# Kernel optimization log

Measured on AMD Instinct MI355X. Metric: run time of the kernel, lower is better.

## Reference

```python
import jax, jax.numpy as jnp
import numpy as np

NUM_Q = 100000; NUM_C = 1000; D = 128; BS = 128; SEQ = 128
QN = 4; CN = 10; NQC = 4; AGG_HOPS = 2; RANK_K = 10
NEG = jnp.float32(-1e9)


def setup_inputs() -> dict:
    key = jax.random.key(0)
    ks = iter(jax.random.split(key, 40))
    def nrm(shape, scale=0.05):
        return jax.random.normal(next(ks), shape, dtype=jnp.float32) * scale
    inp = {}
    inp['question_seq'] = jax.random.randint(next(ks), (BS, SEQ), 0, NUM_Q, dtype=jnp.int32)
    inp['correct_seq'] = jax.random.randint(next(ks), (BS, SEQ), 0, 2, dtype=jnp.int32)
    inp['mask_seq'] = jnp.ones((BS, SEQ), dtype=jnp.int32)
    inp['question_neighbors'] = jax.random.randint(next(ks), (NUM_Q, QN), 0, NUM_C, dtype=jnp.int32)
    inp['concept_neighbors'] = jax.random.randint(next(ks), (NUM_C, CN), 0, NUM_Q, dtype=jnp.int32)
    inp['qc_table'] = jax.random.randint(next(ks), (NUM_Q, NQC), 0, NUM_C, dtype=jnp.int32)
    inp['Eq'] = nrm((NUM_Q, D), 1.0)
    inp['Ec'] = nrm((NUM_C, D), 1.0)
    inp['Er'] = nrm((2, D), 1.0)
    inp['W_ih1'] = nrm((3 * D, 2 * D)); inp['W_hh1'] = nrm((3 * D, D))
    inp['b_ih1'] = nrm((3 * D,)); inp['b_hh1'] = nrm((3 * D,))
    inp['W_ih2'] = nrm((3 * D, D)); inp['W_hh2'] = nrm((3 * D, D))
    inp['b_ih2'] = nrm((3 * D,)); inp['b_hh2'] = nrm((3 * D,))
    inp['W_agg'] = nrm((AGG_HOPS, D, D)); inp['b_agg'] = nrm((AGG_HOPS, D))
    inp['W_agg_last'] = nrm((D, D)); inp['b_agg_last'] = nrm((D,))
    inp['Wq'] = nrm((D, D)); inp['bq'] = nrm((D,))
    inp['Wk'] = nrm((D, D)); inp['bk'] = nrm((D,))
    inp['Ww'] = nrm((1, 2 * D)); inp['bw'] = nrm((1,))
    inp['h1_init'] = nrm((BS, D)); inp['h2_init'] = nrm((BS, D))
    return inp


def _gru(x, h, W_ih, W_hh, b_ih, b_hh):
    gi = x @ W_ih.T + b_ih
    gh = h @ W_hh.T + b_hh
    ir, iz, i_n = jnp.split(gi, 3, axis=-1)
    hr, hz, hn = jnp.split(gh, 3, axis=-1)
    r = jax.nn.sigmoid(ir + hr)
    z = jax.nn.sigmoid(iz + hz)
    n = jnp.tanh(i_n + r * hn)
    return (1 - z) * n + z * h


def _forward(question_seq, correct_seq, mask_seq, question_neighbors, concept_neighbors, qc_table,
             Eq, Ec, Er, W_ih1, W_hh1, b_ih1, b_hh1, W_ih2, W_hh2, b_ih2, b_hh2,
             W_agg, b_agg, W_agg_last, b_agg_last, Wq, bq, Wk, bk, Ww, bw, h1_init, h2_init):
    bs, seq_len = question_seq.shape
    d = Eq.shape[1]
    # detached question embeddings of the whole history (recap scoring key)
    K_all = jax.lax.stop_gradient(Eq[question_seq])  # [bs, seq, d]
    Wh, Wqc = Ww[:, :d], Ww[:, d:]  # MLP_W split over [state; question_concept]

    def predict(qc, hist, hist_mask):
        # qc: [bs,nqc,d], hist: [bs,ns,d], hist_mask: [bs,ns]
        Kp = qc @ Wk.T + bk                     # MLP_key
        Qp = hist @ Wq.T + bq                   # MLP_query
        logits = jnp.einsum('bsd,bqd->bsq', Qp, Kp)
        logits = jnp.where(hist_mask[:, :, None], logits, NEG)
        w = jax.nn.softmax(logits.reshape(bs, -1), axis=1)
        # pairwise sigmoid(MLP_W([h; e])) without materializing the concat
        v = jax.nn.sigmoid((hist @ Wh[0])[:, :, None] + (qc @ Wqc[0])[:, None, :] + bw[0])
        return jnp.sum(w * v.reshape(bs, -1), axis=1)

    def step(carry, t):
        h1, h2, state_hist, y_hat = carry
        q_t = jnp.take(question_seq, t, axis=1)
        r_t = jnp.take(correct_seq, t, axis=1)
        m_t = jnp.take(mask_seq, t, axis=1) != 0
        # --- 2-hop GNN aggregation (question -> concept -> question) ---
        n1 = question_neighbors[q_t]            # [bs, QN] concept ids
        n2 = concept_neighbors[n1]              # [bs, QN, CN] question ids
        emb = [Eq[q_t], Ec[n1], Eq[n2]]
        for i in range(AGG_HOPS):
            for j in range(AGG_HOPS - i):
                s = jnp.mean(emb[j + 1], axis=-2) + emb[j]
                emb[j] = jnp.tanh(s @ W_agg[j].T + b_agg[j])
        agg = jnp.tanh(emb[0] @ W_agg_last.T + b_agg_last)
        emb_q = jnp.where(m_t[:, None], agg, Eq[q_t])
        # --- GRU state updates (dropout in eval mode = identity) ---
        h1n = _gru(jnp.concatenate([emb_q, Er[r_t]], axis=1), h1, W_ih1, W_hh1, b_ih1, b_hh1)
        g2 = _gru(h1n, h2, W_ih2, W_hh2, b_ih2, b_hh2)
        # --- next question + its concepts ---
        q_next = jnp.take(question_seq, t + 1, axis=1)
        qc = jnp.concatenate([Eq[q_next][:, None], Ec[qc_table[q_next]]], axis=1)  # [bs, 1+NQC, d]
        # --- soft recap: top-k history states by detached embedding similarity ---
        scores = jnp.einsum('bsd,bd->bs', K_all, jax.lax.stop_gradient(Eq[q_next]))
        valid = jnp.arange(seq_len) < t
        scores = jnp.where(valid[None, :], scores, NEG)
        top_vals, top_idx = jax.lax.top_k(scores, RANK_K)
        sel = jnp.take_along_axis(state_hist, top_idx[:, :, None], axis=1)  # [bs, k, d]
        sel_mask = top_vals > NEG / 2
        hist = jnp.concatenate([g2[:, None], sel], axis=1)
        hist_mask = jnp.concatenate([jnp.ones((bs, 1), dtype=bool), sel_mask], axis=1)
        p = predict(qc, hist, hist_mask)
        idx = jnp.where(t == 0, 0, t + 1)  # original writes y_hat[:,0] at t==0
        y_hat = y_hat.at[:, idx].set(p)
        # h2 / state_history NOT updated at t==0 (original `continue`)
        upd = t > 0
        h2n = jnp.where(upd, g2, h2)
        state_hist = jnp.where(upd, state_hist.at[:, t].set(g2), state_hist)
        return (h1n, h2n, state_hist, y_hat), None

    init = (h1_init, h2_init,
            jnp.zeros((bs, seq_len, d), jnp.float32),
            jnp.zeros((bs, seq_len), jnp.float32))
    (_, _, _, y_hat), _ = jax.lax.scan(jax.checkpoint(step), init, jnp.arange(seq_len - 1))
    return y_hat


def reference(question_seq, correct_seq, mask_seq, question_neighbors, concept_neighbors, qc_table,
              Eq, Ec, Er, W_ih1, W_hh1, b_ih1, b_hh1, W_ih2, W_hh2, b_ih2, b_hh2,
              W_agg, b_agg, W_agg_last, b_agg_last, Wq, bq, Wk, bk, Ww, bw, h1_init, h2_init):
    return _forward(question_seq, correct_seq, mask_seq, question_neighbors, concept_neighbors, qc_table,
                    Eq, Ec, Er, W_ih1, W_hh1, b_ih1, b_hh1, W_ih2, W_hh2, b_ih2, b_hh2,
                    W_agg, b_agg, W_agg_last, b_agg_last, Wq, bq, Wk, bk, Ww, bw, h1_init, h2_init)
```

## Files before the change

kernel.cpp:

```cpp
#include <hip/hip_runtime.h>

#define DD 128
#define BSZ 128
#define SEQL 128
#define TST 127
#define QNN 4
#define CNN 10
#define NQCC 4
#define RKK 10
#define NEGV -1000000000.0f

#define OFF_WTA0    0
#define OFF_WTA1    16384
#define OFF_WTAL    32768
#define OFF_WTIH1A  49152
#define OFF_ERIH1   98304
#define OFF_MT      99072
#define OFF_WPACK   115456
#define OFF_ECA0    189184
#define OFF_E1C     317184
#define OFF_KQC     445184
#define OFF_VQCC    509184
#define OFF_KBC     510184
#define OFF_U       511184
#define OFF_W2      511312
#define OFF_C0      511440
#define OFF_GRAM    511488
#define OFF_GI1     511488
#define OFF_KQ0     6753792
#define OFF_VQC0    7802368
#define OFF_KB0     7818752
#define OFF_TIX     7835136
#define OFF_TMSK    7997696
#define OFF_CID     8160256

#define XI(e) ((e) + (((e) >> 5) << 2))
#define PH(e) ((((e) >> 5) * 40) + ((e) & 31))
#define PU(e) ((((e) >> 5) * 20) + (((e) & 31) >> 1))

typedef __fp16 h2 __attribute__((ext_vector_type(2)));

__device__ __forceinline__ float sigm(float x) { return 1.0f / (1.0f + __expf(-x)); }
__device__ __forceinline__ float ftanh(float x) {
  float ax = fabsf(x);
  float T = __expf(-2.f * ax);
  float r = (1.f - T) * __builtin_amdgcn_rcpf(1.f + T);
  return copysignf(r, x);
}
__device__ __forceinline__ unsigned pkh(float a, float b) {
  h2 v; v.x = (__fp16)a; v.y = (__fp16)b;
  return __builtin_bit_cast(unsigned, v);
}
__device__ __forceinline__ float fd2(float acc, unsigned w, h2 x) {
  return __builtin_amdgcn_fdot2(__builtin_bit_cast(h2, w), x, acc, false);
}
__device__ __forceinline__ float fd2u(float acc, unsigned w, unsigned x) {
  return __builtin_amdgcn_fdot2(__builtin_bit_cast(h2, w), __builtin_bit_cast(h2, x), acc, false);
}
__device__ __forceinline__ void bar() {
  asm volatile("s_waitcnt lgkmcnt(0)" ::: "memory");
  __builtin_amdgcn_s_barrier();
  asm volatile("" ::: "memory");
}

__global__ __launch_bounds__(256) void k_prep(
    const float* __restrict__ W_hh1, const float* __restrict__ W_ih2,
    const float* __restrict__ W_hh2, const float* __restrict__ W_agg,
    const float* __restrict__ W_agg_last, const float* __restrict__ W_ih1,
    const float* __restrict__ Er, const float* __restrict__ Wq,
    const float* __restrict__ Wk, const float* __restrict__ bq,
    const float* __restrict__ bk, float* __restrict__ ws) {
  int tid = threadIdx.x;
  if (blockIdx.x < 675) {
    int idx = blockIdx.x * 256 + tid;
    const int TOT = 172800;
    for (int o = idx; o < TOT; o += 675 * 256) {
      int r = o;
      if (r < 16384) { int j = r >> 7, i = r & 127; ws[OFF_WTA0 + r] = W_agg[i * 128 + j]; continue; }
      r -= 16384;
      if (r < 16384) { int j = r >> 7, i = r & 127; ws[OFF_WTA1 + r] = W_agg[16384 + i * 128 + j]; continue; }
      r -= 16384;
      if (r < 16384) { int j = r >> 7, i = r & 127; ws[OFF_WTAL + r] = W_agg_last[i * 128 + j]; continue; }
      r -= 16384;
      if (r < 49152) { int j = r / 384, i = r % 384; ws[OFF_WTIH1A + r] = W_ih1[i * 256 + j]; continue; }
      r -= 49152;
      if (r < 768) {
        int rr = r / 384, i2 = r % 384;
        float a = 0.f;
        for (int j = 0; j < 128; ++j) a += Er[rr * 128 + j] * W_ih1[i2 * 256 + 128 + j];
        ws[OFF_ERIH1 + r] = a; continue;
      }
      r -= 768;
      {
        int n = r & 3; int q = r >> 2;
        int i = q & 127; q >>= 7;
        int kk = q & 3; q >>= 2;
        int jc = q & 3; int c = q >> 2;
        int j0 = jc * 32 + kk * 8 + n * 2;
        const float* row;
        if (c < 3) row = W_hh1 + (size_t)(c * 128 + i) * 128;
        else if (c < 6) row = W_ih2 + (size_t)((c - 3) * 128 + i) * 128;
        else row = W_hh2 + (size_t)((c - 6) * 128 + i) * 128;
        ((unsigned*)ws)[OFF_WPACK + r] = pkh(row[j0], row[j0 + 1]);
      }
    }
  } else {
    int j = blockIdx.x - 675;
    __shared__ float wkc[128];
    __shared__ float sc[128];
    if (j < 128) {
      if (tid < 128) wkc[tid] = Wk[tid * 128 + j];
      __syncthreads();
      if (tid < 128) {
        float a = 0.f;
        for (int l = 0; l < 128; ++l) a = fmaf(Wq[l * 128 + tid], wkc[l], a);
        ws[OFF_MT + j * 128 + tid] = a;
      }
    } else if (j == 128) {
      if (tid < 128) {
        float a = 0.f;
        for (int l = 0; l < 128; ++l) a = fmaf(Wq[l * 128 + tid], bk[l], a);
        ws[OFF_U + tid] = a;
      }
    } else {
      if (tid < 128) {
        float a = 0.f;
        for (int l = 0; l < 128; ++l) a = fmaf(bq[l], Wk[l * 128 + tid], a);
        ws[OFF_W2 + tid] = a;
        sc[tid] = bq[tid] * bk[tid];
      }
      __syncthreads();
      if (tid == 0) { float s = 0.f; for (int l = 0; l < 128; ++l) s += sc[l]; ws[OFF_C0] = s; }
    }
  }
}

__global__ __launch_bounds__(128) void k_concept(
    const int* __restrict__ cnbr, const float* __restrict__ Eq,
    const float* __restrict__ Ec, const float* __restrict__ b_agg,
    const float* __restrict__ Ww, float* __restrict__ ws) {
  int c = blockIdx.x;
  int tid = threadIdx.x;
  __shared__ int s_nb[CNN];
  __shared__ float s_v[DD], s_ec[DD], s_t2[DD], s_w2[DD], s_kb2[DD];
  if (tid < CNN) s_nb[tid] = cnbr[c * CNN + tid];
  __syncthreads();
  float ec = Ec[c * DD + tid];
  float cm = 0.f;
#pragma unroll
  for (int l = 0; l < CNN; ++l) cm += Eq[(size_t)s_nb[l] * DD + tid];
  s_ec[tid] = ec;
  s_v[tid] = cm * 0.1f + ec;
  __syncthreads();
  const float* WtA0 = ws + OFF_WTA0;
  const float* WtA1 = ws + OFF_WTA1;
  const float* MT = ws + OFF_MT;
  float a1 = 0.f, a0 = 0.f, kq = 0.f;
#pragma unroll 8
  for (int j = 0; j < DD; ++j) {
    a1 += WtA1[j * DD + tid] * s_v[j];
    a0 += WtA0[j * DD + tid] * s_ec[j];
    kq += MT[j * DD + tid] * s_ec[j];
  }
  ws[OFF_E1C + c * DD + tid] = ftanh(a1 + b_agg[DD + tid]);
  ws[OFF_ECA0 + c * DD + tid] = a0;
  s_t2[tid] = kq + ws[OFF_U + tid];
  s_w2[tid] = s_ec[tid] * Ww[128 + tid];
  s_kb2[tid] = s_ec[tid] * ws[OFF_W2 + tid];
  __syncthreads();
  if (tid < 64) {
    ((unsigned*)ws)[OFF_KQC + c * 64 + tid] = pkh(s_t2[2 * tid], s_t2[2 * tid + 1]);
    float pa = s_w2[tid] + s_w2[tid + 64];
    float pb = s_kb2[tid] + s_kb2[tid + 64];
    for (int off = 32; off > 0; off >>= 1) { pa += __shfl_down(pa, off); pb += __shfl_down(pb, off); }
    if (tid == 0) { ws[OFF_VQCC + c] = pa; ws[OFF_KBC + c] = pb + ws[OFF_C0]; }
  }
}

__global__ __launch_bounds__(256) void k_gram(
    const int* __restrict__ qseq, const float* __restrict__ Eq,
    const float* __restrict__ Ww, float* __restrict__ ws) {
  int role = blockIdx.x >> 7;
  int b = blockIdx.x & 127;
  int tid = threadIdx.x;
  __shared__ float sX[128][129];
  __shared__ int sq[SEQL];
  if (tid < 128) sq[tid] = qseq[b * SEQL + tid];
  __syncthreads();
  for (int o = tid; o < 128 * 32; o += 256) {
    int s = o >> 5, p = o & 31;
    float4 v = ((const float4*)(Eq + (size_t)sq[s] * DD))[p];
    sX[s][p * 4] = v.x; sX[s][p * 4 + 1] = v.y; sX[s][p * 4 + 2] = v.z; sX[s][p * 4 + 3] = v.w;
  }
  __syncthreads();
  if (role == 0) {
    int r0 = (tid >> 4) * 8, c0 = (tid & 15) * 8;
    float acc[8][8];
#pragma unroll
    for (int u = 0; u < 8; ++u)
#pragma unroll
      for (int v = 0; v < 8; ++v) acc[u][v] = 0.f;
    for (int k = 0; k < 128; ++k) {
      float a[8], bb[8];
#pragma unroll
      for (int u = 0; u < 8; ++u) { a[u] = sX[r0 + u][k]; bb[u] = sX[c0 + u][k]; }
#pragma unroll
      for (int u = 0; u < 8; ++u)
#pragma unroll
        for (int v = 0; v < 8; ++v) acc[u][v] = fmaf(a[u], bb[v], acc[u][v]);
    }
    float* gb = ws + OFF_GRAM + (size_t)b * 16384;
#pragma unroll
    for (int u = 0; u < 8; ++u) {
      float4 v0 = {acc[u][0], acc[u][1], acc[u][2], acc[u][3]};
      float4 v1 = {acc[u][4], acc[u][5], acc[u][6], acc[u][7]};
      ((float4*)(gb + (size_t)(r0 + u) * 128 + c0))[0] = v0;
      ((float4*)(gb + (size_t)(r0 + u) * 128 + c0 + 4))[0] = v1;
    }
  } else {
    __shared__ float s_tmp[2][8][DD];
    __shared__ float sU[DD], sWqc[DD], sW2[DD];
    if (tid < 128) {
      sU[tid] = ws[OFF_U + tid];
      sWqc[tid] = Ww[128 + tid];
      sW2[tid] = ws[OFF_W2 + tid];
    }
    __syncthreads();
    const float* MT = ws + OFF_MT;
    unsigned* KQ0 = (unsigned*)ws + OFF_KQ0;
    int i = tid & 127, half = tid >> 7;
    int s0 = half * 64;
    for (int sb = 0; sb < 64; sb += 8) {
      float acc[8];
#pragma unroll
      for (int u = 0; u < 8; ++u) acc[u] = 0.f;
      for (int j = 0; j < DD; ++j) {
        float w = MT[j * DD + i];
#pragma unroll
        for (int u = 0; u < 8; ++u) acc[u] = fmaf(w, sX[s0 + sb + u][j], acc[u]);
      }
      __syncthreads();
#pragma unroll
      for (int u = 0; u < 8; ++u) s_tmp[half][u][i] = acc[u] + sU[i];
      __syncthreads();
      for (int o = tid; o < 16 * 64; o += 256) {
        int rr = o >> 6, e = o & 63;
        int hh = rr >> 3, uu = rr & 7;
        int s = hh * 64 + sb + uu;
        KQ0[((size_t)b * 128 + s) * 64 + e] = pkh(s_tmp[hh][uu][2 * e], s_tmp[hh][uu][2 * e + 1]);
      }
      __syncthreads();
    }
    if (tid < 128) {
      float a = 0.f, kb = 0.f;
      for (int j = 0; j < DD; ++j) {
        float xv = sX[tid][j];
        a = fmaf(xv, sWqc[j], a);
        kb = fmaf(xv, sW2[j], kb);
      }
      ws[OFF_VQC0 + b * 128 + tid] = a;
      ws[OFF_KB0 + b * 128 + tid] = kb + ws[OFF_C0];
    }
  }
}

__global__ __launch_bounds__(128) void k_topk(
    const int* __restrict__ qseq, const int* __restrict__ qctab,
    float* __restrict__ ws) {
  int* tix = (int*)(ws + OFF_TIX);
  int* tmsk = (int*)(ws + OFF_TMSK);
  int* cid = (int*)(ws + OFF_CID);
  int tid = threadIdx.x;
  int lane = tid & 63, wv = tid >> 6;
  int bt = blockIdx.x * 2 + wv;
  int b = bt / TST, t = bt - b * TST;
  if (lane < 5) {
    int qn = qseq[b * SEQL + t + 1];
    cid[(b * 128 + t + 1) * 5 + lane] = (lane == 0) ? qn : qctab[qn * NQCC + lane - 1];
  }
  const float* grow = ws + OFF_GRAM + ((size_t)b * 128 + (t + 1)) * 128;
  float v0 = (lane < t) ? grow[lane] : NEGV;
  float v1 = (lane + 64 < t) ? grow[lane + 64] : NEGV;
  for (int k = 0; k < RKK; ++k) {
    float bv = v0; int bi = lane;
    if (v1 > bv) { bv = v1; bi = lane + 64; }
    for (int off = 32; off > 0; off >>= 1) {
      float ov = __shfl_down(bv, off);
      int oi = __shfl_down(bi, off);
      if (ov > bv || (ov == bv && oi < bi)) { bv = ov; bi = oi; }
    }
    bv = __shfl(bv, 0); bi = __shfl(bi, 0);
    if (lane == 0) {
      tix[bt * RKK + k] = bi;
      tmsk[bt * RKK + k] = (bv > NEGV * 0.5f) ? 1 : 0;
    }
    if (bi == lane) v0 = -__builtin_inff();
    if (bi == lane + 64) v1 = -__builtin_inff();
  }
}

__global__ __launch_bounds__(128) void k_agg(
    const int* __restrict__ qseq, const int* __restrict__ rseq,
    const int* __restrict__ mseq, const int* __restrict__ qnbr,
    const float* __restrict__ Eq, const float* __restrict__ b_agg,
    const float* __restrict__ b_agg_last, const float* __restrict__ b_ih1,
    float* __restrict__ ws) {
  int blk = blockIdx.x;
  int b = blk >> 4, g = blk & 15;
  int t0 = g * 8;
  int nu = (t0 + 8 <= TST) ? 8 : (TST - t0);
  int tid = threadIdx.x;
  __shared__ float s_a[8][DD], s_b[8][DD], s_c[8][DD];
  __shared__ int s_q[8], s_r[8], s_m[8];
  __shared__ int s_n1[8][QNN];
  if (tid < 8) {
    int ok = tid < nu;
    int idx = b * SEQL + (ok ? (t0 + tid) : 0);
    s_q[tid] = qseq[idx];
    s_r[tid] = ok ? rseq[idx] : 0;
    s_m[tid] = ok ? mseq[idx] : 0;
  }
  __syncthreads();
  if (tid < 32) { int u = tid >> 2, k = tid & 3; s_n1[u][k] = qnbr[s_q[u] * QNN + k]; }
  for (int o = tid; o < 8 * 32; o += 128) {
    int u = o >> 5, p = o & 31;
    float4 v = ((const float4*)(Eq + (size_t)s_q[u] * DD))[p];
    s_a[u][p * 4] = v.x; s_a[u][p * 4 + 1] = v.y; s_a[u][p * 4 + 2] = v.z; s_a[u][p * 4 + 3] = v.w;
  }
  __syncthreads();
  const float* WtA0 = ws + OFF_WTA0;
  const float* WtAL = ws + OFF_WTAL;
  const float* WtIH1A = ws + OFF_WTIH1A;
  const float* EcA0 = ws + OFF_ECA0;
  const float* E1C = ws + OFF_E1C;
  float acc[8];
#pragma unroll
  for (int u = 0; u < 8; ++u) acc[u] = 0.f;
  for (int j = 0; j < DD; ++j) {
    float w = WtA0[j * DD + tid];
#pragma unroll
    for (int u = 0; u < 8; ++u) acc[u] = fmaf(w, s_a[u][j], acc[u]);
  }
  float bat = b_agg[tid];
#pragma unroll
  for (int u = 0; u < 8; ++u) {
    int n0 = s_n1[u][0], n1 = s_n1[u][1], n2 = s_n1[u][2], n3 = s_n1[u][3];
    float pre0 = 0.25f * (EcA0[n0 * DD + tid] + EcA0[n1 * DD + tid] + EcA0[n2 * DD + tid] + EcA0[n3 * DD + tid]);
    float e0 = ftanh(acc[u] + pre0 + bat);
    float e1m = 0.25f * (E1C[n0 * DD + tid] + E1C[n1 * DD + tid] + E1C[n2 * DD + tid] + E1C[n3 * DD + tid]);
    s_b[u][tid] = e1m + e0;
  }
  __syncthreads();
#pragma unroll
  for (int u = 0; u < 8; ++u) acc[u] = 0.f;
  for (int j = 0; j < DD; ++j) {
    float w = WtA0[j * DD + tid];
#pragma unroll
    for (int u = 0; u < 8; ++u) acc[u] = fmaf(w, s_b[u][j], acc[u]);
  }
#pragma unroll
  for (int u = 0; u < 8; ++u) s_c[u][tid] = ftanh(acc[u] + bat);
  __syncthreads();
#pragma unroll
  for (int u = 0; u < 8; ++u) acc[u] = 0.f;
  for (int j = 0; j < DD; ++j) {
    float w = WtAL[j * DD + tid];
#pragma unroll
    for (int u = 0; u < 8; ++u) acc[u] = fmaf(w, s_c[u][j], acc[u]);
  }
  float balt = b_agg_last[tid];
#pragma unroll
  for (int u = 0; u < 8; ++u) {
    float aggv = ftanh(acc[u] + balt);
    s_b[u][tid] = s_m[u] ? aggv : s_a[u][tid];
  }
  __syncthreads();
  float g0[8], g1[8], g2[8];
#pragma unroll
  for (int u = 0; u < 8; ++u) { g0[u] = 0.f; g1[u] = 0.f; g2[u] = 0.f; }
  for (int j = 0; j < DD; ++j) {
    float w0 = WtIH1A[j * 384 + tid];
    float w1 = WtIH1A[j * 384 + 128 + tid];
    float w2 = WtIH1A[j * 384 + 256 + tid];
#pragma unroll
    for (int u = 0; u < 8; ++u) {
      float x = s_b[u][j];
      g0[u] = fmaf(w0, x, g0[u]);
      g1[u] = fmaf(w1, x, g1[u]);
      g2[u] = fmaf(w2, x, g2[u]);
    }
  }
  for (int u = 0; u < nu; ++u) {
    const float* ErI = ws + OFF_ERIH1 + s_r[u] * 384;
    float* gi1 = ws + OFF_GI1 + (size_t)(b * TST + t0 + u) * 384;
    gi1[tid] = g0[u] + ErI[tid] + b_ih1[tid];
    gi1[128 + tid] = g1[u] + ErI[128 + tid] + b_ih1[128 + tid];
    gi1[256 + tid] = g2[u] + ErI[256 + tid] + b_ih1[256 + tid];
  }
}

__global__ __launch_bounds__(512, 2) void k_seq(
    const float* __restrict__ b_hh1, const float* __restrict__ b_ih2,
    const float* __restrict__ b_hh2, const float* __restrict__ Ww,
    const float* __restrict__ bw, const float* __restrict__ h1i,
    const float* __restrict__ h2i, float* __restrict__ ws,
    float* __restrict__ out) {
  const int tid = threadIdx.x;
  const int b = blockIdx.x;
  const int i = tid >> 2, jc = tid & 3;
  const int lane = tid & 63, wv = tid >> 6;
  const int bt0 = b * TST;

  const float4* gi1f4 = (const float4*)(ws + OFF_GI1);
  const unsigned* KQ0 = (const unsigned*)ws + OFF_KQ0;
  const unsigned* KQC = (const unsigned*)ws + OFF_KQC;
  const float* vqc0_all = ws + OFF_VQC0;
  const float* vqcC_all = ws + OFF_VQCC;
  const float* kb0_all = ws + OFF_KB0;
  const float* kbC_all = ws + OFF_KBC;
  const int* tix_all = (const int*)(ws + OFF_TIX);
  const int* tmsk_all = (const int*)(ws + OFF_TMSK);
  const int* cid_all = (const int*)(ws + OFF_CID);
  const uint4* wp = (const uint4*)((const unsigned*)ws + OFF_WPACK);

  __shared__ float s_h1f[2][144], s_g2f[2][144], s_h2f[144];
  __shared__ unsigned s_h1pk[2][80], s_g2pk[2][80], s_h2pk[80];
  __shared__ unsigned qph_pk[SEQL * 66];
  __shared__ unsigned s_Kq[2][5 * 66];
  __shared__ float s_gi1[384];
  __shared__ float s_vhh[SEQL];
  __shared__ float s_logit[64];
  __shared__ float s_bhh1[384], s_bih2[384], s_bhh2[384];
  __shared__ float s_vh[11], s_vqc[2][5], s_kb[2][5], s_bw;
  __shared__ int s_tix[RKK], s_hm[11], s_cidn[5];

  uint4 wgt[9][4];
#pragma unroll
  for (int c = 0; c < 9; ++c)
#pragma unroll
    for (int kk = 0; kk < 4; ++kk)
      wgt[c][kk] = wp[((c * 4 + jc) * 4 + kk) * 128 + i];
#pragma unroll
  for (int c = 0; c < 9; ++c)
#pragma unroll
    for (int kk = 0; kk < 4; ++kk)
      asm volatile("" : "+v"(wgt[c][kk].x), "+v"(wgt[c][kk].y),
                        "+v"(wgt[c][kk].z), "+v"(wgt[c][kk].w));

  if (tid < 384) { s_bhh1[tid] = b_hh1[tid]; s_bih2[tid] = b_ih2[tid]; s_bhh2[tid] = b_hh2[tid]; }
  if (tid < 128) {
    float h1v = h1i[b * DD + tid], h2v = h2i[b * DD + tid];
    s_h1f[0][XI(tid)] = h1v;
    ((__fp16*)s_h1pk[0])[PH(tid)] = (__fp16)h1v;
    s_h2f[XI(tid)] = h2v;
    ((__fp16*)s_h2pk)[PH(tid)] = (__fp16)h2v;
    s_vhh[tid] = 0.f;
  }
  if (tid >= 55 && tid < 64) s_logit[tid] = NEGV;
  float wh_lo = 0.f, wh_hi = 0.f;
  if (wv == 7) { wh_lo = Ww[lane]; wh_hi = Ww[64 + lane]; }
  if (tid == 0) { s_bw = bw[0]; out[b * SEQL + 1] = 0.f; s_hm[0] = 1; }
  if (tid >= 296 && tid < 301) s_cidn[tid - 296] = cid_all[(b * 128 + 1) * 5 + tid - 296];
  __syncthreads();
  for (int o = tid; o < SEQL * 66; o += 512) qph_pk[o] = 0u;
  if (tid < 96) ((float4*)s_gi1)[tid] = gi1f4[(size_t)bt0 * 96 + tid];
  __syncthreads();

  for (int t = 0; t <= TST; ++t) {
    const int par = t & 1, parn = par ^ 1;
    float4 pf4 = {0.f, 0.f, 0.f, 0.f};
    unsigned pfu = 0, pfu2 = 0; int pfs = 0; float pfv = 0.f, pfkb = 0.f;

    if (t < TST) {
      const int tg = (t + 1 < TST) ? t + 1 : TST - 1;
      if (tid < 96) pf4 = gi1f4[(size_t)(bt0 + tg) * 96 + tid];
      else if (tid < 256) {
        int kx = tid - 96;
        { int s = kx >> 6, e = kx & 63;
          pfu = (s == 0) ? KQ0[(size_t)(b * 128 + t + 1) * 64 + e] : KQC[s_cidn[s] * 64 + e]; }
        { int kx2 = kx + 160; int s = kx2 >> 6, e = kx2 & 63;
          pfu2 = KQC[s_cidn[s] * 64 + e]; }
      } else if (tid < 291) {
        int k = tid - 256;
        if (k < 5) pfv = (k == 0) ? vqc0_all[b * 128 + t + 1] : vqcC_all[s_cidn[k]];
        else if (k < 10) { int s = k - 5; pfkb = (s == 0) ? kb0_all[b * 128 + t + 1] : kbC_all[s_cidn[s]]; }
        else if (k < 20) pfs = tix_all[(bt0 + t) * RKK + k - 10];
        else if (k < 30) pfs = tmsk_all[(bt0 + t) * RKK + k - 20];
        else { int tn = (t + 1 < TST) ? t + 1 : TST - 1; pfs = cid_all[(b * 128 + tn + 1) * 5 + k - 30]; }
      }
      const uint4* xp = (const uint4*)s_h1pk[par] + jc * 5;
      float a0 = 0.f, a1 = 0.f, a2 = 0.f;
#pragma unroll
      for (int kk = 0; kk < 4; ++kk) {
        uint4 xk = xp[kk];
        uint4 w;
        w = wgt[0][kk]; a0 = fd2u(a0, w.x, xk.x); a0 = fd2u(a0, w.y, xk.y); a0 = fd2u(a0, w.z, xk.z); a0 = fd2u(a0, w.w, xk.w);
        w = wgt[1][kk]; a1 = fd2u(a1, w.x, xk.x); a1 = fd2u(a1, w.y, xk.y); a1 = fd2u(a1, w.z, xk.z); a1 = fd2u(a1, w.w, xk.w);
        w = wgt[2][kk]; a2 = fd2u(a2, w.x, xk.x); a2 = fd2u(a2, w.y, xk.y); a2 = fd2u(a2, w.z, xk.z); a2 = fd2u(a2, w.w, xk.w);
      }
      a0 += __shfl_down(a0, 2); a0 += __shfl_down(a0, 1);
      a1 += __shfl_down(a1, 2); a1 += __shfl_down(a1, 1);
      a2 += __shfl_down(a2, 2); a2 += __shfl_down(a2, 1);
      if (jc == 0) {
        float r = sigm(s_gi1[i] + a0 + s_bhh1[i]);
        float z = sigm(s_gi1[128 + i] + a1 + s_bhh1[128 + i]);
        float n = ftanh(s_gi1[256 + i] + r * (a2 + s_bhh1[256 + i]));
        float h1n = (1.f - z) * n + z * s_h1f[par][XI(i)];
        s_h1f[parn][XI(i)] = h1n;
        ((__fp16*)s_h1pk[parn])[PH(i)] = (__fp16)h1n;
      }
    }
    if (t >= 1) {
      if (tid < 440) {
        int p = tid >> 3, sub = tid & 7;
        int q = p / 5, s = p - q * 5;
        const unsigned* kpr = &s_Kq[parn][s * 66 + sub * 8];
        float a = 0.f;
        if (q == 0) {
          const unsigned* g2u = s_g2pk[parn];
          int e0 = sub * 16;
#pragma unroll
          for (int k = 0; k < 8; ++k) a = fd2u(a, kpr[k], g2u[PU(e0 + 2 * k)]);
        } else {
          const unsigned* ro = qph_pk + s_tix[q - 1] * 66;
#pragma unroll
          for (int k = 0; k < 8; ++k) a = fd2u(a, ro[sub * 8 + k], kpr[k]);
        }
        a += __shfl_down(a, 4);
        a += __shfl_down(a, 2);
        a += __shfl_down(a, 1);
        if (sub == 0) s_logit[p] = s_hm[q] ? (a + s_kb[parn][s]) : NEGV;
      } else if (wv == 7) {
        float pa = s_g2f[parn][XI(lane)] * wh_lo + s_g2f[parn][XI(64 + lane)] * wh_hi;
        for (int off = 32; off > 0; off >>= 1) pa += __shfl_down(pa, off);
        if (lane == 0) s_vh[0] = pa;
        if (lane >= 16 && lane < 26) s_vh[1 + lane - 16] = s_vhh[s_tix[lane - 16]];
      }
    }
    bar();

    if (t < TST) {
      const uint4* xn = (const uint4*)s_h1pk[parn] + jc * 5;
      const uint4* xh = (t <= 1) ? ((const uint4*)s_h2pk + jc * 5)
                                 : ((const uint4*)s_g2pk[parn] + jc * 5);
      float a0 = 0.f, a1 = 0.f, a2 = 0.f, c0 = 0.f, c1 = 0.f, c2 = 0.f;
#pragma unroll
      for (int kk = 0; kk < 4; ++kk) {
        uint4 xa = xn[kk], xb = xh[kk];
        uint4 w;
        w = wgt[3][kk]; a0 = fd2u(a0, w.x, xa.x); a0 = fd2u(a0, w.y, xa.y); a0 = fd2u(a0, w.z, xa.z); a0 = fd2u(a0, w.w, xa.w);
        w = wgt[4][kk]; a1 = fd2u(a1, w.x, xa.x); a1 = fd2u(a1, w.y, xa.y); a1 = fd2u(a1, w.z, xa.z); a1 = fd2u(a1, w.w, xa.w);
        w = wgt[5][kk]; a2 = fd2u(a2, w.x, xa.x); a2 = fd2u(a2, w.y, xa.y); a2 = fd2u(a2, w.z, xa.z); a2 = fd2u(a2, w.w, xa.w);
        w = wgt[6][kk]; c0 = fd2u(c0, w.x, xb.x); c0 = fd2u(c0, w.y, xb.y); c0 = fd2u(c0, w.z, xb.z); c0 = fd2u(c0, w.w, xb.w);
        w = wgt[7][kk]; c1 = fd2u(c1, w.x, xb.x); c1 = fd2u(c1, w.y, xb.y); c1 = fd2u(c1, w.z, xb.z); c1 = fd2u(c1, w.w, xb.w);
        w = wgt[8][kk]; c2 = fd2u(c2, w.x, xb.x); c2 = fd2u(c2, w.y, xb.y); c2 = fd2u(c2, w.z, xb.z); c2 = fd2u(c2, w.w, xb.w);
      }
      a0 += __shfl_down(a0, 2); a0 += __shfl_down(a0, 1);
      a1 += __shfl_down(a1, 2); a1 += __shfl_down(a1, 1);
      a2 += __shfl_down(a2, 2); a2 += __shfl_down(a2, 1);
      c0 += __shfl_down(c0, 2); c0 += __shfl_down(c0, 1);
      c1 += __shfl_down(c1, 2); c1 += __shfl_down(c1, 1);
      c2 += __shfl_down(c2, 2); c2 += __shfl_down(c2, 1);
      if (jc == 0) {
        float r = sigm(a0 + s_bih2[i] + c0 + s_bhh2[i]);
        float z = sigm(a1 + s_bih2[128 + i] + c1 + s_bhh2[128 + i]);
        float n = ftanh(a2 + s_bih2[256 + i] + r * (c2 + s_bhh2[256 + i]));
        float h2old = (t <= 1) ? s_h2f[XI(i)] : s_g2f[parn][XI(i)];
        float g2v = (1.f - z) * n + z * h2old;
        s_g2f[par][XI(i)] = g2v;
        ((__fp16*)s_g2pk[par])[PH(i)] = (__fp16)g2v;
      }
    }
    if (t >= 1 && wv == 7) {
      float l = s_logit[lane];
      float m = l;
      for (int off = 32; off > 0; off >>= 1) m = fmaxf(m, __shfl_xor(m, off));
      float e = __expf(l - m);
      float v = 0.f;
      if (lane < 55) {
        int q = lane / 5, s = lane - q * 5;
        v = sigm(s_vh[q] + s_vqc[parn][s] + s_bw);
      }
      float num = e * v, den = e;
      for (int off = 32; off > 0; off >>= 1) { num += __shfl_xor(num, off); den += __shfl_xor(den, off); }
      if (lane == 0) out[b * SEQL + ((t - 1 == 0) ? 0 : t)] = num / den;
    }
    if (t < TST) {
      if (tid < 96) ((float4*)s_gi1)[tid] = pf4;
      else if (tid < 256) {
        int kx = tid - 96;
        { int s = kx >> 6, e = kx & 63; s_Kq[par][s * 66 + e] = pfu; }
        { int kx2 = kx + 160; int s = kx2 >> 6, e = kx2 & 63; s_Kq[par][s * 66 + e] = pfu2; }
      } else if (tid < 291) {
        int k = tid - 256;
        if (k < 5) s_vqc[par][k] = pfv;
        else if (k < 10) s_kb[par][k - 5] = pfkb;
        else if (k < 20) s_tix[k - 10] = pfs;
        else if (k < 30) s_hm[1 + k - 20] = pfs;
        else s_cidn[k - 30] = pfs;
      }
    }
    if (t >= 2 && tid >= 320 && tid < 384) {
      int k2 = tid - 320;
      qph_pk[(t - 1) * 66 + k2] = s_g2pk[parn][PU(2 * k2)];
    }
    if (t >= 2 && tid == 0) s_vhh[t - 1] = s_vh[0];
    bar();
  }
}

extern "C" void kernel_launch(void* const* d_in, const int* in_sizes, int n_in,
                              void* d_out, int out_size, void* d_ws, size_t ws_size,
                              hipStream_t stream) {
  (void)in_sizes; (void)n_in; (void)out_size; (void)ws_size;
  const int* qseq = (const int*)d_in[0];
  const int* rseq = (const int*)d_in[1];
  const int* mseq = (const int*)d_in[2];
  const int* qnbr = (const int*)d_in[3];
  const int* cnbr = (const int*)d_in[4];
  const int* qctab = (const int*)d_in[5];
  const float* Eq = (const float*)d_in[6];
  const float* Ec = (const float*)d_in[7];
  const float* Er = (const float*)d_in[8];
  const float* W_ih1 = (const float*)d_in[9];
  const float* W_hh1 = (const float*)d_in[10];
  const float* b_ih1 = (const float*)d_in[11];
  const float* b_hh1 = (const float*)d_in[12];
  const float* W_ih2 = (const float*)d_in[13];
  const float* W_hh2 = (const float*)d_in[14];
  const float* b_ih2 = (const float*)d_in[15];
  const float* b_hh2 = (const float*)d_in[16];
  const float* W_agg = (const float*)d_in[17];
  const float* b_agg = (const float*)d_in[18];
  const float* W_agg_last = (const float*)d_in[19];
  const float* b_agg_last = (const float*)d_in[20];
  const float* Wq = (const float*)d_in[21];
  const float* bq = (const float*)d_in[22];
  const float* Wk = (const float*)d_in[23];
  const float* bk = (const float*)d_in[24];
  const float* Ww = (const float*)d_in[25];
  const float* bw = (const float*)d_in[26];
  const float* h1i = (const float*)d_in[27];
  const float* h2i = (const float*)d_in[28];
  float* ws = (float*)d_ws;
  float* out = (float*)d_out;

  hipLaunchKernelGGL(k_prep, dim3(805), dim3(256), 0, stream,
                     W_hh1, W_ih2, W_hh2, W_agg, W_agg_last, W_ih1, Er,
                     Wq, Wk, bq, bk, ws);
  hipLaunchKernelGGL(k_concept, dim3(1000), dim3(128), 0, stream,
                     cnbr, Eq, Ec, b_agg, Ww, ws);
  hipLaunchKernelGGL(k_gram, dim3(256), dim3(256), 0, stream,
                     qseq, Eq, Ww, ws);
  hipLaunchKernelGGL(k_topk, dim3(BSZ * TST / 2), dim3(128), 0, stream,
                     qseq, qctab, ws);
  hipLaunchKernelGGL(k_agg, dim3(BSZ * 16), dim3(128), 0, stream,
                     qseq, rseq, mseq, qnbr, Eq, b_agg, b_agg_last, b_ih1, ws);
  hipLaunchKernelGGL(k_seq, dim3(BSZ), dim3(512), 0, stream,
                     b_hh1, b_ih2, b_hh2, Ww, bw, h1i, h2i, ws, out);
}
```

Baseline: 574.4 us.

## Fuse top-k selection into gram kernel using shared-memory gram matrix

The separate top-k kernel is removed. The gram matrix now stays in shared memory inside k_gram, and each block's four waves run the top-10 selection over the rows directly. The concept-id table writes move into the other role of k_gram. This removes a kernel launch and the 8 MB gram round trip through global memory. In exchange, the top-k work now runs serially over only 128 blocks of 4 waves each instead of 8128 wave-sized blocks, and the extra shared memory may lower occupancy.

```diff
diff --git a/kernel.cpp b/kernel.cpp
--- a/kernel.cpp
+++ b/kernel.cpp
@@ -25,7 +25,6 @@
 #define OFF_U       511184
 #define OFF_W2      511312
 #define OFF_C0      511440
-#define OFF_GRAM    511488
 #define OFF_GI1     511488
 #define OFF_KQ0     6753792
 #define OFF_VQC0    7802368
@@ -50,9 +49,6 @@
 __device__ __forceinline__ unsigned pkh(float a, float b) {
   h2 v; v.x = (__fp16)a; v.y = (__fp16)b;
   return __builtin_bit_cast(unsigned, v);
-}
-__device__ __forceinline__ float fd2(float acc, unsigned w, h2 x) {
-  return __builtin_amdgcn_fdot2(__builtin_bit_cast(h2, w), x, acc, false);
 }
 __device__ __forceinline__ float fd2u(float acc, unsigned w, unsigned x) {
   return __builtin_amdgcn_fdot2(__builtin_bit_cast(h2, w), __builtin_bit_cast(h2, x), acc, false);
@@ -178,11 +174,13 @@
 }
 
 __global__ __launch_bounds__(256) void k_gram(
-    const int* __restrict__ qseq, const float* __restrict__ Eq,
-    const float* __restrict__ Ww, float* __restrict__ ws) {
+    const int* __restrict__ qseq, const int* __restrict__ qctab,
+    const float* __restrict__ Eq, const float* __restrict__ Ww,
+    float* __restrict__ ws) {
   int role = blockIdx.x >> 7;
   int b = blockIdx.x & 127;
   int tid = threadIdx.x;
+  int lane = tid & 63, wv = tid >> 6;
   __shared__ float sX[128][129];
   __shared__ int sq[SEQL];
   if (tid < 128) sq[tid] = qseq[b * SEQL + tid];
@@ -194,6 +192,7 @@
   }
   __syncthreads();
   if (role == 0) {
+    __shared__ float sGram[128][130];
     int r0 = (tid >> 4) * 8, c0 = (tid & 15) * 8;
     float acc[8][8];
 #pragma unroll
@@ -209,13 +208,34 @@
 #pragma unroll
         for (int v = 0; v < 8; ++v) acc[u][v] = fmaf(a[u], bb[v], acc[u][v]);
     }
-    float* gb = ws + OFF_GRAM + (size_t)b * 16384;
-#pragma unroll
-    for (int u = 0; u < 8; ++u) {
-      float4 v0 = {acc[u][0], acc[u][1], acc[u][2], acc[u][3]};
-      float4 v1 = {acc[u][4], acc[u][5], acc[u][6], acc[u][7]};
-      ((float4*)(gb + (size_t)(r0 + u) * 128 + c0))[0] = v0;
-      ((float4*)(gb + (size_t)(r0 + u) * 128 + c0 + 4))[0] = v1;
+#pragma unroll
+    for (int u = 0; u < 8; ++u)
+#pragma unroll
+      for (int v = 0; v < 8; ++v) sGram[r0 + u][c0 + v] = acc[u][v];
+    __syncthreads();
+    int* tix = (int*)(ws + OFF_TIX);
+    int* tmsk = (int*)(ws + OFF_TMSK);
+    for (int t = wv; t < TST; t += 4) {
+      const float* grow = sGram[t + 1];
+      float v0 = (lane < t) ? grow[lane] : NEGV;
+      float v1 = (lane + 64 < t) ? grow[lane + 64] : NEGV;
+      int bt = b * TST + t;
+      for (int k = 0; k < RKK; ++k) {
+        float bv = v0; int bi = lane;
+        if (v1 > bv) { bv = v1; bi = lane + 64; }
+        for (int off = 32; off > 0; off >>= 1) {
+          float ov = __shfl_down(bv, off);
+          int oi = __shfl_down(bi, off);
+          if (ov > bv || (ov == bv && oi < bi)) { bv = ov; bi = oi; }
+        }
+        bv = __shfl(bv, 0); bi = __shfl(bi, 0);
+        if (lane == 0) {
+          tix[bt * RKK + k] = bi;
+          tmsk[bt * RKK + k] = (bv > NEGV * 0.5f) ? 1 : 0;
+        }
+        if (bi == lane) v0 = -__builtin_inff();
+        if (bi == lane + 64) v1 = -__builtin_inff();
+      }
     }
   } else {
     __shared__ float s_tmp[2][8][DD];
@@ -225,6 +245,14 @@
       sWqc[tid] = Ww[128 + tid];
       sW2[tid] = ws[OFF_W2 + tid];
     }
+    {
+      int* cid = (int*)(ws + OFF_CID);
+      for (int o = tid; o < 127 * 5; o += 256) {
+        int tp = 1 + o / 5, k = o - (o / 5) * 5;
+        int qn = sq[tp];
+        cid[(b * 128 + tp) * 5 + k] = (k == 0) ? qn : qctab[qn * NQCC + k - 1];
+      }
+    }
     __syncthreads();
     const float* MT = ws + OFF_MT;
     unsigned* KQ0 = (unsigned*)ws + OFF_KQ0;
@@ -261,41 +289,6 @@
       ws[OFF_VQC0 + b * 128 + tid] = a;
       ws[OFF_KB0 + b * 128 + tid] = kb + ws[OFF_C0];
     }
-  }
-}
-
-__global__ __launch_bounds__(128) void k_topk(
-    const int* __restrict__ qseq, const int* __restrict__ qctab,
-    float* __restrict__ ws) {
-  int* tix = (int*)(ws + OFF_TIX);
-  int* tmsk = (int*)(ws + OFF_TMSK);
-  int* cid = (int*)(ws + OFF_CID);
-  int tid = threadIdx.x;
-  int lane = tid & 63, wv = tid >> 6;
-  int bt = blockIdx.x * 2 + wv;
-  int b = bt / TST, t = bt - b * TST;
-  if (lane < 5) {
-    int qn = qseq[b * SEQL + t + 1];
-    cid[(b * 128 + t + 1) * 5 + lane] = (lane == 0) ? qn : qctab[qn * NQCC + lane - 1];
-  }
-  const float* grow = ws + OFF_GRAM + ((size_t)b * 128 + (t + 1)) * 128;
-  float v0 = (lane < t) ? grow[lane] : NEGV;
-  float v1 = (lane + 64 < t) ? grow[lane + 64] : NEGV;
-  for (int k = 0; k < RKK; ++k) {
-    float bv = v0; int bi = lane;
-    if (v1 > bv) { bv = v1; bi = lane + 64; }
-    for (int off = 32; off > 0; off >>= 1) {
-      float ov = __shfl_down(bv, off);
-      int oi = __shfl_down(bi, off);
-      if (ov > bv || (ov == bv && oi < bi)) { bv = ov; bi = oi; }
-    }
-    bv = __shfl(bv, 0); bi = __shfl(bi, 0);
-    if (lane == 0) {
-      tix[bt * RKK + k] = bi;
-      tmsk[bt * RKK + k] = (bv > NEGV * 0.5f) ? 1 : 0;
-    }
-    if (bi == lane) v0 = -__builtin_inff();
-    if (bi == lane + 64) v1 = -__builtin_inff();
   }
 }
 
@@ -651,9 +644,7 @@
   hipLaunchKernelGGL(k_concept, dim3(1000), dim3(128), 0, stream,
                      cnbr, Eq, Ec, b_agg, Ww, ws);
   hipLaunchKernelGGL(k_gram, dim3(256), dim3(256), 0, stream,
-                     qseq, Eq, Ww, ws);
-  hipLaunchKernelGGL(k_topk, dim3(BSZ * TST / 2), dim3(128), 0, stream,
-                     qseq, qctab, ws);
+                     qseq, qctab, Eq, Ww, ws);
   hipLaunchKernelGGL(k_agg, dim3(BSZ * 16), dim3(128), 0, stream,
                      qseq, rseq, mseq, qnbr, Eq, b_agg, b_agg_last, b_ih1, ws);
   hipLaunchKernelGGL(k_seq, dim3(BSZ), dim3(512), 0, stream,
```

Result: slower. 684.2 us (+19.1%).
